# Performance work log

Measured on AMD Instinct MI355X. Metric: run time of the kernel, lower is better.

The kernel has to match this reference:

```python
import jax, jax.numpy as jnp
import numpy as np

B, F, D = 1024, 256, 64  # batch, featureNumb, featureDim


def setup_inputs() -> dict:
    key = jax.random.key(0)
    k1, k2, k3, k4 = jax.random.split(key, 4)
    feature = jax.random.normal(k1, (B, F, D), dtype=jnp.float32)
    indicator = jax.random.normal(k2, (F, D), dtype=jnp.float32)
    # QKVTransformV2(n, D, D): n stacked DxD linear maps of the indicator
    W_qk = jax.random.normal(k3, (2, D, D), dtype=jnp.float32) / np.float32(np.sqrt(D))
    W_qkv = jax.random.normal(k4, (3, D, D), dtype=jnp.float32) / np.float32(np.sqrt(D))
    return {"feature": feature, "indicator": indicator, "W_qk": W_qk, "W_qkv": W_qkv}


def reference(feature, indicator, W_qk, W_qkv):
    d = indicator.shape[-1]
    scale = jnp.asarray(1.0 / np.sqrt(d), feature.dtype)

    # --- gate branch: QKTrans + DotWeight + LTE (straight-through hard threshold) ---
    trans = jnp.einsum('fd,nde->nfe', indicator, W_qk)            # [2,F,D]
    gate_logits = jnp.einsum('id,jd->ij', trans[0], trans[1]) * scale  # [F,F]
    gate = (gate_logits > 0).astype(feature.dtype)                # LTE forward: hard 0/1 gate

    # --- QKV branch, fused form of the rank-1 outer products ---
    # Original: QKV_outer[t,i,j] = qkv[t,i] (x) qkv[t,j]  (DxD rank-1)
    #           input[b,t,i,j,:] = feature[b,i] @ QKV_outer[t,i,j]
    #                            = (feature[b,i] . qkv[t,i]) * qkv[t,j]
    qkv = jnp.einsum('fd,nde->nfe', indicator, W_qkv)             # [3,F,D]
    s = jnp.einsum('bfd,nfd->nbf', feature, qkv)                  # s[t,b,i] = feature[b,i].qkv[t,i]

    # score[b,i,j] = input[b,0,i,j,:] . input[b,1,j,i,:]
    #              = s[0,b,i] * s[1,b,j] * (qkv[1,i] . qkv[0,j])
    cross = jnp.einsum('id,jd->ij', qkv[1], qkv[0])               # [F,F]
    score = s[0][:, :, None] * s[1][:, None, :] * cross[None]     # [B,F,F]
    scoreHat = score * gate[None]                                 # [B,F,F]

    # output[b,i,:] = sum_j scoreHat[b,i,j] * value[b,i,j,:]
    #               = s[2,b,i] * sum_j scoreHat[b,i,j] * qkv[2,j,:]
    out = s[2][:, :, None] * jnp.einsum('bij,jd->bid', scoreHat, qkv[2])  # [B,F,D]
    return out
```

## Files before the change

### kernel.cpp

```cpp
#include <hip/hip_runtime.h>
#include <stdint.h>

#define B 1024
#define F 256
#define D 64

typedef __attribute__((ext_vector_type(8))) short short8;
typedef __attribute__((ext_vector_type(4))) float f32x4;

typedef __attribute__((address_space(1))) const unsigned GU;
typedef __attribute__((address_space(3))) unsigned LU;

__device__ __forceinline__ short f2bf(float f) {
    unsigned u = __builtin_bit_cast(unsigned, f);
    u += 0x7fff + ((u >> 16) & 1);
    return (short)(u >> 16);
}
__device__ __forceinline__ float bf2f(short s) {
    unsigned u = ((unsigned)(unsigned short)s) << 16;
    return __builtin_bit_cast(float, u);
}


__global__ void precompute_trans(const float* __restrict__ indicator,
                                 const float* __restrict__ W_qk,
                                 const float* __restrict__ W_qkv,
                                 float* __restrict__ trans,
                                 float* __restrict__ qkv) {
    int idx = blockIdx.x * blockDim.x + threadIdx.x;
    int n   = idx / (F * D);
    int rem = idx - n * (F * D);
    int f   = rem / D;
    int e   = rem - f * D;
    const float* W = (n < 2) ? (W_qk + n * D * D) : (W_qkv + (n - 2) * D * D);
    const float* ind = indicator + f * D;
    float acc = 0.f;
#pragma unroll 8
    for (int d = 0; d < D; ++d) acc += ind[d] * W[d * D + e];
    if (n < 2) trans[n * F * D + f * D + e] = acc;
    else       qkv[(n - 2) * F * D + f * D + e] = acc;
}

__global__ void compute_Mt(const float* __restrict__ trans,
                           const float* __restrict__ qkv,
                           short* __restrict__ At,
                           short* __restrict__ q2T) {
    int j = blockIdx.x;
    int i = threadIdx.x;
    const float* t0 = trans + i * D;
    const float* t1 = trans + F * D + j * D;
    const float* q1 = qkv + F * D + i * D;
    const float* q0 = qkv + j * D;
    float d0 = 0.f, d1 = 0.f;
#pragma unroll 8
    for (int d = 0; d < D; ++d) {
        d0 += t0[d] * t1[d];
        d1 += q1[d] * q0[d];
    }
    float v = (d0 > 0.f) ? d1 : 0.f;
    At[((j >> 5) * F + i) * 32 + (j & 31)] = f2bf(v);
    if (j < D) q2T[j * F + i] = f2bf(qkv[2 * F * D + i * D + j]);
}

__global__ __launch_bounds__(256) void compute_s(const float* __restrict__ feature,
                                                 const float* __restrict__ qkv,
                                                 float* __restrict__ s0,
                                                 float* __restrict__ s1,
                                                 float* __restrict__ s2) {
    int g   = blockIdx.x * 256 + threadIdx.x;
    int row = g >> 4;
    int l   = g & 15;
    int f   = row & (F - 1);
    float4 fv = ((const float4*)(feature + (size_t)row * D))[l];
    float4 q0 = ((const float4*)(qkv + f * D))[l];
    float4 q1 = ((const float4*)(qkv + F * D + f * D))[l];
    float4 q2 = ((const float4*)(qkv + 2 * F * D + f * D))[l];
    float p0 = fv.x * q0.x + fv.y * q0.y + fv.z * q0.z + fv.w * q0.w;
    float p1 = fv.x * q1.x + fv.y * q1.y + fv.z * q1.z + fv.w * q1.w;
    float p2 = fv.x * q2.x + fv.y * q2.y + fv.z * q2.z + fv.w * q2.w;
#pragma unroll
    for (int m = 1; m < 16; m <<= 1) {
        p0 += __shfl_xor(p0, m, 64);
        p1 += __shfl_xor(p1, m, 64);
        p2 += __shfl_xor(p2, m, 64);
    }
    if (l == 0) {
        s0[row] = p0;
        s1[row] = p1;
        s2[row] = p2;
    }
}

__global__ __launch_bounds__(256) void main_mfma(const short* __restrict__ At,
                                                 const short* __restrict__ q2T,
                                                 const float* __restrict__ s0,
                                                 const float* __restrict__ s1,
                                                 const float* __restrict__ s2,
                                                 float* __restrict__ out) {
    int blk = blockIdx.x;
    int ih  = blk & 1;
    int bp  = blk >> 1;
    int b0  = bp * 2;
    int i0  = ih * 128;

    __shared__ short As[128 * 32];
    __shared__ short Bs[128 * 32];
    __shared__ float s1s[2 * F];
    __shared__ float gs[2 * 128];

    int tid = threadIdx.x;

    s1s[tid]       = s1[b0 * F + tid];
    s1s[F + tid]   = s1[(b0 + 1) * F + tid];
    {
        int bl = tid >> 7, il = tid & 127;
        int r  = (b0 + bl) * F + i0 + il;
        gs[tid] = s0[r] * s2[r];
    }

    int wave = tid >> 6;
    int lane = tid & 63;
    int wr = wave >> 1, wc = wave & 1;
    int l16 = lane & 15;
    int lq  = lane >> 4;

    f32x4 acc[4][4];
#pragma unroll
    for (int mt = 0; mt < 4; ++mt)
#pragma unroll
        for (int nt = 0; nt < 4; ++nt) acc[mt][nt] = (f32x4){0.f, 0.f, 0.f, 0.f};

    for (int jt = 0; jt < F / 32; ++jt) {
        __syncthreads();
        {
            const char* gA = (const char*)(At + ((size_t)jt * F + i0) * 32);
            __builtin_amdgcn_global_load_lds((GU*)(gA + tid * 16),
                                             (LU*)((char*)As + tid * 16), 16, 0, 0);
            __builtin_amdgcn_global_load_lds((GU*)(gA + 4096 + tid * 16),
                                             (LU*)((char*)As + 4096 + tid * 16), 16, 0, 0);
        }
        {
            int n  = tid & 127;
            int jh = tid >> 7;
            int d  = n & 63, bl = n >> 6;
            const short* q  = q2T + d * F + jt * 32 + jh * 16;
            const float* sv = s1s + bl * F + jt * 32 + jh * 16;
            short* bd = Bs + n * 32 + jh * 16;
#pragma unroll
            for (int k = 0; k < 16; ++k) bd[k] = f2bf(bf2f(q[k]) * sv[k]);
        }
        __syncthreads();
        short8 af[4], bf[4];
        const short* aBase = As + ((wr * 64 + l16) * 32) + lq * 8;
        const short* bBase = Bs + ((wc * 64 + l16) * 32) + lq * 8;
#pragma unroll
        for (int mt = 0; mt < 4; ++mt) af[mt] = *(const short8*)(aBase + mt * 16 * 32);
#pragma unroll
        for (int nt = 0; nt < 4; ++nt) bf[nt] = *(const short8*)(bBase + nt * 16 * 32);
#pragma unroll
        for (int mt = 0; mt < 4; ++mt)
#pragma unroll
            for (int nt = 0; nt < 4; ++nt)
                acc[mt][nt] = __builtin_amdgcn_mfma_f32_16x16x32_bf16(
                    af[mt], bf[nt], acc[mt][nt], 0, 0, 0);
    }

    int b = b0 + wc;
#pragma unroll
    for (int mt = 0; mt < 4; ++mt) {
#pragma unroll
        for (int r = 0; r < 4; ++r) {
            int i_loc = wr * 64 + mt * 16 + lq * 4 + r;
            float g = gs[wc * 128 + i_loc];
            float* orow = out + ((size_t)(b * F + i0 + i_loc)) * D;
#pragma unroll
            for (int nt = 0; nt < 4; ++nt)
                orow[nt * 16 + l16] = g * acc[mt][nt][r];
        }
    }
}

extern "C" void kernel_launch(void* const* d_in, const int* in_sizes, int n_in,
                              void* d_out, int out_size, void* d_ws, size_t ws_size,
                              hipStream_t stream) {
    const float* feature   = (const float*)d_in[0];
    const float* indicator = (const float*)d_in[1];
    const float* W_qk      = (const float*)d_in[2];
    const float* W_qkv     = (const float*)d_in[3];
    float* out = (float*)d_out;

    float* ws    = (float*)d_ws;
    float* trans = ws;
    float* qkv   = trans + 2 * F * D;
    float* s0    = qkv + 3 * F * D;
    float* s1    = s0 + B * F;
    float* s2    = s1 + B * F;
    short* At    = (short*)(s2 + B * F);
    short* q2T   = At + F * F;

    hipLaunchKernelGGL(precompute_trans, dim3((5 * F * D) / 256), dim3(256), 0,
                       stream, indicator, W_qk, W_qkv, trans, qkv);
    hipLaunchKernelGGL(compute_Mt, dim3(F), dim3(F), 0, stream, trans, qkv, At, q2T);
    hipLaunchKernelGGL(compute_s, dim3(B * F * 16 / 256), dim3(256), 0, stream,
                       feature, qkv, s0, s1, s2);
    hipLaunchKernelGGL(main_mfma, dim3(B), dim3(256), 0, stream, At, q2T,
                       s0, s1, s2, out);
}
```

Baseline: 147.9 us.

## Drop LDS staging in main MFMA kernel; load fragments directly from global

```diff
diff --git a/kernel.cpp b/kernel.cpp
--- a/kernel.cpp
+++ b/kernel.cpp
@@ -8,9 +8,6 @@
 typedef __attribute__((ext_vector_type(8))) short short8;
 typedef __attribute__((ext_vector_type(4))) float f32x4;
 
-typedef __attribute__((address_space(1))) const unsigned GU;
-typedef __attribute__((address_space(3))) unsigned LU;
-
 __device__ __forceinline__ short f2bf(float f) {
     unsigned u = __builtin_bit_cast(unsigned, f);
     u += 0x7fff + ((u >> 16) & 1);
@@ -19,6 +16,11 @@
 __device__ __forceinline__ float bf2f(short s) {
     unsigned u = ((unsigned)(unsigned short)s) << 16;
     return __builtin_bit_cast(float, u);
+}
+__device__ __forceinline__ unsigned pk_bf16(float a, float b) {
+    unsigned ua = __builtin_bit_cast(unsigned, a) + 0x8000u;
+    unsigned ub = __builtin_bit_cast(unsigned, b) + 0x8000u;
+    return __builtin_amdgcn_perm(ub, ua, 0x07060302u);
 }
 
 
@@ -41,35 +43,35 @@
     else       qkv[(n - 2) * F * D + f * D + e] = acc;
 }
 
-__global__ void compute_Mt(const float* __restrict__ trans,
-                           const float* __restrict__ qkv,
-                           short* __restrict__ At,
-                           short* __restrict__ q2T) {
+__global__ __launch_bounds__(256) void compute_Mt(const float* __restrict__ trans,
+                                                  const float* __restrict__ qkv,
+                                                  short* __restrict__ At,
+                                                  short* __restrict__ q2K) {
     int j = blockIdx.x;
     int i = threadIdx.x;
-    const float* t0 = trans + i * D;
-    const float* t1 = trans + F * D + j * D;
-    const float* q1 = qkv + F * D + i * D;
-    const float* q0 = qkv + j * D;
+    const float4* t0 = (const float4*)(trans + i * D);
+    const float4* t1 = (const float4*)(trans + F * D + j * D);
+    const float4* q1 = (const float4*)(qkv + F * D + i * D);
+    const float4* q0 = (const float4*)(qkv + j * D);
     float d0 = 0.f, d1 = 0.f;
-#pragma unroll 8
-    for (int d = 0; d < D; ++d) {
-        d0 += t0[d] * t1[d];
-        d1 += q1[d] * q0[d];
+#pragma unroll
+    for (int k = 0; k < D / 4; ++k) {
+        float4 a = t0[k], b = t1[k], c = q1[k], e = q0[k];
+        d0 += a.x * b.x + a.y * b.y + a.z * b.z + a.w * b.w;
+        d1 += c.x * e.x + c.y * e.y + c.z * e.z + c.w * e.w;
     }
     float v = (d0 > 0.f) ? d1 : 0.f;
     At[((j >> 5) * F + i) * 32 + (j & 31)] = f2bf(v);
-    if (j < D) q2T[j * F + i] = f2bf(qkv[2 * F * D + i * D + j]);
+    if (j < D) q2K[((i >> 5) * D + j) * 32 + (i & 31)] = f2bf(qkv[2 * F * D + i * D + j]);
 }
 
 __global__ __launch_bounds__(256) void compute_s(const float* __restrict__ feature,
                                                  const float* __restrict__ qkv,
-                                                 float* __restrict__ s0,
-                                                 float* __restrict__ s1,
-                                                 float* __restrict__ s2) {
-    int g   = blockIdx.x * 256 + threadIdx.x;
-    int row = g >> 4;
-    int l   = g & 15;
+                                                 float* __restrict__ g,
+                                                 short* __restrict__ s1b) {
+    int gid = blockIdx.x * 256 + threadIdx.x;
+    int row = gid >> 4;
+    int l   = gid & 15;
     int f   = row & (F - 1);
     float4 fv = ((const float4*)(feature + (size_t)row * D))[l];
     float4 q0 = ((const float4*)(qkv + f * D))[l];
@@ -85,17 +87,15 @@
         p2 += __shfl_xor(p2, m, 64);
     }
     if (l == 0) {
-        s0[row] = p0;
-        s1[row] = p1;
-        s2[row] = p2;
+        g[row]   = p0 * p2;
+        s1b[row] = f2bf(p1);
     }
 }
 
 __global__ __launch_bounds__(256) void main_mfma(const short* __restrict__ At,
-                                                 const short* __restrict__ q2T,
-                                                 const float* __restrict__ s0,
-                                                 const float* __restrict__ s1,
-                                                 const float* __restrict__ s2,
+                                                 const short* __restrict__ q2K,
+                                                 const short* __restrict__ s1b,
+                                                 const float* __restrict__ g,
                                                  float* __restrict__ out) {
     int blk = blockIdx.x;
     int ih  = blk & 1;
@@ -103,26 +103,13 @@
     int b0  = bp * 2;
     int i0  = ih * 128;
 
-    __shared__ short As[128 * 32];
-    __shared__ short Bs[128 * 32];
-    __shared__ float s1s[2 * F];
-    __shared__ float gs[2 * 128];
-
-    int tid = threadIdx.x;
-
-    s1s[tid]       = s1[b0 * F + tid];
-    s1s[F + tid]   = s1[(b0 + 1) * F + tid];
-    {
-        int bl = tid >> 7, il = tid & 127;
-        int r  = (b0 + bl) * F + i0 + il;
-        gs[tid] = s0[r] * s2[r];
-    }
-
+    int tid  = threadIdx.x;
     int wave = tid >> 6;
     int lane = tid & 63;
-    int wr = wave >> 1, wc = wave & 1;
-    int l16 = lane & 15;
-    int lq  = lane >> 4;
+    int wr   = wave >> 1, wc = wave & 1;
+    int l16  = lane & 15;
+    int lq   = lane >> 4;
+    int b    = b0 + wc;
 
     f32x4 acc[4][4];
 #pragma unroll
@@ -131,32 +118,30 @@
         for (int nt = 0; nt < 4; ++nt) acc[mt][nt] = (f32x4){0.f, 0.f, 0.f, 0.f};
 
     for (int jt = 0; jt < F / 32; ++jt) {
-        __syncthreads();
-        {
-            const char* gA = (const char*)(At + ((size_t)jt * F + i0) * 32);
-            __builtin_amdgcn_global_load_lds((GU*)(gA + tid * 16),
-                                             (LU*)((char*)As + tid * 16), 16, 0, 0);
-            __builtin_amdgcn_global_load_lds((GU*)(gA + 4096 + tid * 16),
-                                             (LU*)((char*)As + 4096 + tid * 16), 16, 0, 0);
+        int kq = lq * 8;
+        short8 sv = *(const short8*)(s1b + b * F + jt * 32 + kq);
+        float sf[8];
+#pragma unroll
+        for (int e = 0; e < 8; ++e) sf[e] = bf2f(sv[e]);
+
+        short8 af[4];
+#pragma unroll
+        for (int mt = 0; mt < 4; ++mt) {
+            int i = i0 + wr * 64 + mt * 16 + l16;
+            af[mt] = *(const short8*)(At + (jt * F + i) * 32 + kq);
         }
-        {
-            int n  = tid & 127;
-            int jh = tid >> 7;
-            int d  = n & 63, bl = n >> 6;
-            const short* q  = q2T + d * F + jt * 32 + jh * 16;
-            const float* sv = s1s + bl * F + jt * 32 + jh * 16;
-            short* bd = Bs + n * 32 + jh * 16;
+        short8 bf[4];
 #pragma unroll
-            for (int k = 0; k < 16; ++k) bd[k] = f2bf(bf2f(q[k]) * sv[k]);
+        for (int nt = 0; nt < 4; ++nt) {
+            int d = nt * 16 + l16;
+            short8 qv = *(const short8*)(q2K + (jt * D + d) * 32 + kq);
+            int4 packed;
+            packed.x = pk_bf16(bf2f(qv[0]) * sf[0], bf2f(qv[1]) * sf[1]);
+            packed.y = pk_bf16(bf2f(qv[2]) * sf[2], bf2f(qv[3]) * sf[3]);
+            packed.z = pk_bf16(bf2f(qv[4]) * sf[4], bf2f(qv[5]) * sf[5]);
+            packed.w = pk_bf16(bf2f(qv[6]) * sf[6], bf2f(qv[7]) * sf[7]);
+            bf[nt] = __builtin_bit_cast(short8, packed);
         }
-        __syncthreads();
-        short8 af[4], bf[4];
-        const short* aBase = As + ((wr * 64 + l16) * 32) + lq * 8;
-        const short* bBase = Bs + ((wc * 64 + l16) * 32) + lq * 8;
-#pragma unroll
-        for (int mt = 0; mt < 4; ++mt) af[mt] = *(const short8*)(aBase + mt * 16 * 32);
-#pragma unroll
-        for (int nt = 0; nt < 4; ++nt) bf[nt] = *(const short8*)(bBase + nt * 16 * 32);
 #pragma unroll
         for (int mt = 0; mt < 4; ++mt)
 #pragma unroll
@@ -165,17 +150,16 @@
                     af[mt], bf[nt], acc[mt][nt], 0, 0, 0);
     }
 
-    int b = b0 + wc;
 #pragma unroll
     for (int mt = 0; mt < 4; ++mt) {
 #pragma unroll
         for (int r = 0; r < 4; ++r) {
             int i_loc = wr * 64 + mt * 16 + lq * 4 + r;
-            float g = gs[wc * 128 + i_loc];
+            float gg = g[b * F + i0 + i_loc];
             float* orow = out + ((size_t)(b * F + i0 + i_loc)) * D;
 #pragma unroll
             for (int nt = 0; nt < 4; ++nt)
-                orow[nt * 16 + l16] = g * acc[mt][nt][r];
+                orow[nt * 16 + l16] = gg * acc[mt][nt][r];
         }
     }
 }
@@ -192,17 +176,16 @@
     float* ws    = (float*)d_ws;
     float* trans = ws;
     float* qkv   = trans + 2 * F * D;
-    float* s0    = qkv + 3 * F * D;
-    float* s1    = s0 + B * F;
-    float* s2    = s1 + B * F;
-    short* At    = (short*)(s2 + B * F);
-    short* q2T   = At + F * F;
+    float* g     = qkv + 3 * F * D;
+    short* At    = (short*)(g + B * F);
+    short* q2K   = At + F * F;
+    short* s1b   = q2K + (F / 32) * D * 32;
 
     hipLaunchKernelGGL(precompute_trans, dim3((5 * F * D) / 256), dim3(256), 0,
                        stream, indicator, W_qk, W_qkv, trans, qkv);
-    hipLaunchKernelGGL(compute_Mt, dim3(F), dim3(F), 0, stream, trans, qkv, At, q2T);
+    hipLaunchKernelGGL(compute_Mt, dim3(F), dim3(F), 0, stream, trans, qkv, At, q2K);
     hipLaunchKernelGGL(compute_s, dim3(B * F * 16 / 256), dim3(256), 0, stream,
-                       feature, qkv, s0, s1, s2);
-    hipLaunchKernelGGL(main_mfma, dim3(B), dim3(256), 0, stream, At, q2T,
-                       s0, s1, s2, out);
+                       feature, qkv, g, s1b);
+    hipLaunchKernelGGL(main_mfma, dim3(B), dim3(256), 0, stream, At, q2K,
+                       s1b, g, out);
 }
```

New measurement: 148.4 us. About the same (+0.4%).
